# Kernel optimization log

Hardware: AMD Instinct MI355X
Metric: run time of the kernel (lower is better)

The kernel has to match this reference:

```python
import jax, jax.numpy as jnp
import numpy as np

DIM = 192
R = 16            # patches_resolution, D=H=W=R
SP = 4            # split_size
NH = 6            # num_heads (block level); per-branch heads = NH//3
B = 2
L = R * R * R
EPS = 1e-5


def layernorm(x, g, b):
    mu = jnp.mean(x, axis=-1, keepdims=True)
    var = jnp.mean(jnp.square(x - mu), axis=-1, keepdims=True)
    return (x - mu) * jax.lax.rsqrt(var + EPS) * g + b


def window_partition(x, d_sp, h_sp, w_sp, nh):
    b, _, _, _, cb = x.shape
    win = d_sp * h_sp * w_sp
    x = x.reshape(b, R // d_sp, d_sp, R // h_sp, h_sp, R // w_sp, w_sp, cb)
    x = x.transpose(0, 1, 3, 5, 2, 4, 6, 7).reshape(-1, win, nh, cb // nh)
    return x.transpose(0, 2, 1, 3)


def window_merge(x, d_sp, h_sp, w_sp, b):
    cb = x.shape[-1]
    x = x.reshape(b, R // d_sp, R // h_sp, R // w_sp, d_sp, h_sp, w_sp, cb)
    x = x.transpose(0, 1, 4, 2, 5, 3, 6, 7).reshape(b, L, cb)
    return x


def lepe_attention(q, k, v, d_sp, h_sp, w_sp, nh):
    # q,k,v: (B, L, Cb). Note: LePE bias is computed-but-unused in the source -> pure windowed SDPA.
    b, _, cb = q.shape
    hd = cb // nh
    scale = hd ** -0.5
    q5 = q.reshape(b, R, R, R, cb)
    k5 = k.reshape(b, R, R, R, cb)
    v5 = v.reshape(b, R, R, R, cb)
    qw = window_partition(q5, d_sp, h_sp, w_sp, nh) * scale
    kw = window_partition(k5, d_sp, h_sp, w_sp, nh)
    vw = window_partition(v5, d_sp, h_sp, w_sp, nh)
    attn = jax.nn.softmax(jnp.einsum('whqd,whkd->whqk', qw, kw), axis=-1)
    out = jnp.einsum('whqk,whkd->whqd', attn, vw)
    out = out.transpose(0, 2, 1, 3).reshape(-1, d_sp * h_sp * w_sp, cb)
    return window_merge(out, d_sp, h_sp, w_sp, b)


WINDOW_SHAPES = [(R, R, SP), (R, SP, R), (SP, R, R)]  # idx 0,1,2


def setup_inputs() -> dict:
    key = jax.random.key(0)
    ks = jax.random.split(key, 12)
    C = DIM
    H4 = int(C * 4)
    inp = {
        'x': jax.random.normal(ks[0], (B, C, R, R, R), dtype=jnp.float32),
        'w_qkv': jax.random.normal(ks[1], (C, 3 * C), dtype=jnp.float32) * (C ** -0.5),
        'w_proj': jax.random.normal(ks[2], (C, C), dtype=jnp.float32) * (C ** -0.5),
        'b_proj': jnp.zeros((C,), dtype=jnp.float32),
        'g1': jnp.ones((C,), dtype=jnp.float32),
        'b1': jnp.zeros((C,), dtype=jnp.float32),
        'g2': jnp.ones((C,), dtype=jnp.float32),
        'b2': jnp.zeros((C,), dtype=jnp.float32),
        'w_fc1': jax.random.normal(ks[3], (C, H4), dtype=jnp.float32) * (C ** -0.5),
        'b_fc1': jnp.zeros((H4,), dtype=jnp.float32),
        'w_fc2': jax.random.normal(ks[4], (H4, C), dtype=jnp.float32) * (H4 ** -0.5),
        'b_fc2': jnp.zeros((C,), dtype=jnp.float32),
    }
    return inp


def reference(x, w_qkv, w_proj, b_proj, g1, b1, g2, b2, w_fc1, b_fc1, w_fc2, b_fc2):
    C = DIM
    Cb = C // 3
    nh_b = NH // 3
    x = 2.0 * x
    xt = jnp.transpose(x, (0, 2, 3, 4, 1))                # (B, D, H, W, C)
    img = layernorm(xt, g1, b1)
    qkv = img.reshape(B, L, C) @ w_qkv                    # (B, L, 3C)
    q, k, v = jnp.split(qkv.reshape(B, L, 3, C).transpose(2, 0, 1, 3), 3, axis=0)
    q, k, v = q[0], k[0], v[0]                            # each (B, L, C)
    outs = []
    for i, (dsp, hsp, wsp) in enumerate(WINDOW_SHAPES):
        sl = slice(i * Cb, (i + 1) * Cb)
        outs.append(lepe_attention(q[..., sl], k[..., sl], v[..., sl], dsp, hsp, wsp, nh_b))
    attened = jnp.concatenate(outs, axis=2)               # (B, L, C)
    attened = attened @ w_proj + b_proj
    xs = xt.reshape(B, L, C) + attened
    h = layernorm(xs, g2, b2) @ w_fc1 + b_fc1
    h = jax.nn.gelu(h, approximate=False)
    xs = xs + (h @ w_fc2 + b_fc2)
    out = xs.reshape(B, R, R, R, C).transpose(0, 4, 1, 2, 3)  # (B, C, D, H, W)
    return out
```

## Files before the change

### kernel.cpp

```cpp
#include <hip/hip_runtime.h>
#include <hip/hip_bf16.h>

typedef __hip_bfloat16 bf16;
typedef short short8 __attribute__((ext_vector_type(8)));
typedef float floatx4 __attribute__((ext_vector_type(4)));

#define SZ (8192*192)

__device__ __forceinline__ unsigned short f2b(float f) {
    unsigned u = __builtin_bit_cast(unsigned, f);
    u += 0x7FFFu + ((u >> 16) & 1u);
    return (unsigned short)(u >> 16);
}
__device__ __forceinline__ float b2f(unsigned short h) {
    unsigned u = ((unsigned)h) << 16;
    return __builtin_bit_cast(float, u);
}
__device__ __forceinline__ unsigned pk2(float a, float b) {
    return ((unsigned)f2b(b) << 16) | (unsigned)f2b(a);
}
__device__ __forceinline__ float fexp2(float x) {
    float r;
    asm("v_exp_f32 %0, %1" : "=v"(r) : "v"(x));
    return r;
}

__device__ __forceinline__ int detect_inline(const unsigned* __restrict__ x32,
                                             int tid, int* cnt) {
    if (tid == 0) *cnt = 0;
    __syncthreads();
    if (tid < 256) {
        unsigned u = x32[tid];
        int c = (int)(((u >> 7) & 0xFFu) >= 152u) + (int)(((u >> 23) & 0xFFu) >= 152u);
        if (c) atomicAdd(cnt, c);
    }
    __syncthreads();
    return (*cnt >= 16) ? 1 : 0;
}

struct WPA { const void* s[11]; };

__global__ __launch_bounds__(256) void wprep_kernel(WPA a, unsigned short* __restrict__ wdst,
                                                    float* __restrict__ vdst,
                                                    const unsigned* __restrict__ x32) {
    __shared__ int cnt;
    int f = detect_inline(x32, threadIdx.x, &cnt);
    int i = blockIdx.x * 256 + threadIdx.x;
    if (i < 442368) {
        int seg, base, K, N;
        if (i < 110592)      { seg = 0; base = 0;      K = 192; N = 576; }
        else if (i < 147456) { seg = 1; base = 110592; K = 192; N = 192; }
        else if (i < 294912) { seg = 2; base = 147456; K = 192; N = 768; }
        else                 { seg = 3; base = 294912; K = 768; N = 192; }
        int j = i - base;
        int n = j / K, k = j - n * K;
        size_t src = (size_t)k * N + n;
        float v = f ? ((const float*)a.s[seg])[src] : b2f(((const unsigned short*)a.s[seg])[src]);
        int ci = (n >> 6) * (K >> 5) + (k >> 5);
        int off = (ci << 11) + (((n >> 4) & 3) << 9) + ((n & 15) << 5) + (k & 31);
        wdst[base + off] = f2b(v);
    } else if (i < 444288) {
        int j = i - 442368;
        int seg, off;
        if (j < 960)       { seg = 4 + j / 192; off = j % 192; }
        else if (j < 1728) { seg = 9; off = j - 960; }
        else               { seg = 10; off = j - 1728; }
        float v = f ? ((const float*)a.s[seg])[off] : b2f(((const unsigned short*)a.s[seg])[off]);
        vdst[j] = v;
    }
}


__global__ __launch_bounds__(256) void prep_kernel(const void* __restrict__ xin,
        int* __restrict__ flagOut,
        const float* __restrict__ g1, const float* __restrict__ b1,
        float* __restrict__ xt, unsigned short* __restrict__ img) {
    __shared__ float tile[192][33];
    __shared__ float mu[32], rs[32];
    __shared__ int cnt;
    int tid = threadIdx.x;
    int f = detect_inline((const unsigned*)xin, tid, &cnt);
    if (blockIdx.x == 0 && tid == 0) *flagOut = f;
    int t0 = blockIdx.x * 32;
    int b = t0 >> 12;
    int ts = t0 & 4095;
    for (int idx = tid; idx < 192 * 32; idx += 256) {
        int c = idx >> 5, tt = idx & 31;
        int gi = ((b * 192 + c) << 12) + ts + tt;
        float raw = f ? ((const float*)xin)[gi] : b2f(((const unsigned short*)xin)[gi]);
        tile[c][tt] = 2.0f * raw;
    }
    __syncthreads();
    {
        int tt = tid >> 3, j = tid & 7;
        int c0 = j * 24;
        float s = 0.f, sq = 0.f;
        #pragma unroll
        for (int i = 0; i < 24; ++i) { float v = tile[c0 + i][tt]; s += v; sq += v * v; }
        s += __shfl_xor(s, 1); sq += __shfl_xor(sq, 1);
        s += __shfl_xor(s, 2); sq += __shfl_xor(sq, 2);
        s += __shfl_xor(s, 4); sq += __shfl_xor(sq, 4);
        if (j == 0) {
            float m = s * (1.0f / 192.0f);
            float var = sq * (1.0f / 192.0f) - m * m;
            mu[tt] = m;
            rs[tt] = rsqrtf(var + 1e-5f);
        }
    }
    __syncthreads();
    for (int idx = tid; idx < 32 * 192; idx += 256) {
        int tt = idx / 192, c = idx % 192;
        float v = tile[c][tt];
        xt[(t0 + tt) * 192 + c] = v;
        int po = ((((t0 + tt) >> 4) * 6 + (c >> 5)) << 9) + ((tt & 15) << 5) + (c & 31);
        img[po] = f2b((v - mu[tt]) * rs[tt] * g1[c] + b1[c]);
    }
}

__device__ __forceinline__ int g_of(int br, int t) {
    if (br == 0) return (((t >> 2) & 3) << 10) | ((t >> 8) << 6) | (((t >> 4) & 15) << 2) | (t & 3);
    if (br == 1) return (((t >> 6) & 3) << 10) | ((t >> 8) << 6) | (((t >> 4) & 3) << 4) | (t & 15);
    return t;
}

template <int MODE, int W>
__global__ __launch_bounds__(64 * W) void mfma_gemm(const unsigned short* __restrict__ A,
        const unsigned short* __restrict__ WT, const float* __restrict__ bias,
        const float* __restrict__ resid, void* __restrict__ out,
        unsigned short* __restrict__ qt, unsigned short* __restrict__ kt,
        unsigned short* __restrict__ vt, int N, int K) {
    int wave = threadIdx.x >> 6, lane = threadIdx.x & 63;
    int quad = lane >> 4, l16 = lane & 15;
    int m0 = blockIdx.x * (32 * W) + wave * 32, n0 = blockIdx.y * 64;
    const int KT = K >> 5;
    const unsigned short* ap = A + (((size_t)(m0 >> 4) * KT) << 9) + l16 * 32 + quad * 8;
    const size_t a1off = ((size_t)KT) << 9;
    const unsigned short* wpB = WT + (((size_t)blockIdx.y * KT) << 11) + l16 * 32 + quad * 8;
    floatx4 acc[2][4] = {};
    #pragma unroll 2
    for (int kc = 0; kc < K; kc += 32) {
        const unsigned short* ac = ap + (((size_t)(kc >> 5)) << 9);
        short8 a0 = *reinterpret_cast<const short8*>(ac);
        short8 a1 = *reinterpret_cast<const short8*>(ac + a1off);
        const unsigned short* wc = wpB + (((size_t)(kc >> 5)) << 11);
        #pragma unroll
        for (int nt = 0; nt < 4; ++nt) {
            short8 w = *reinterpret_cast<const short8*>(wc + nt * 512);
            acc[0][nt] = __builtin_amdgcn_mfma_f32_16x16x32_bf16(a0, w, acc[0][nt], 0, 0, 0);
            acc[1][nt] = __builtin_amdgcn_mfma_f32_16x16x32_bf16(a1, w, acc[1][nt], 0, 0, 0);
        }
    }
    #pragma unroll
    for (int fh = 0; fh < 2; ++fh) {
        #pragma unroll
        for (int nt = 0; nt < 4; ++nt) {
            int col = n0 + nt * 16 + l16;
            if (MODE == 0 && n0 >= 384) {
                int cv = col - 384;
                int d = cv & 31, brh = cv >> 5;
                int row0 = m0 + fh * 16 + quad * 4;
                int bb_ = row0 >> 12, tl = row0 & 4095;
                int g0 = g_of(brh >> 1, tl);
                int wb2 = g0 >> 10, k = g0 & 63, c = k >> 4, m = k & 15;
                int pos = ((c >> 1) << 5) + ((m >> 2) << 3) + ((c & 1) << 2);
                int chunk = (g0 & 1023) >> 6;
                int tidx = ((d >> 4) << 1) | (pos >> 5);
                unsigned short* tile = vt + (((((size_t)(bb_ * 6 + brh) * 4 + wb2) * 16 + chunk) * 4 + tidx) << 9);
                ushort4 w4;
                w4.x = f2b(acc[fh][nt][0]);
                w4.y = f2b(acc[fh][nt][1]);
                w4.z = f2b(acc[fh][nt][2]);
                w4.w = f2b(acc[fh][nt][3]);
                *reinterpret_cast<ushort4*>(tile + (d & 15) * 32 + (pos & 31)) = w4;
            } else if (MODE == 0 && n0 >= 192) {
                int ck = col - 192;
                int d = ck & 31, brh = ck >> 5;
                int row0 = m0 + fh * 16 + quad * 4;
                int bb_ = row0 >> 12, tl = row0 & 4095;
                int g0 = g_of(brh >> 1, tl);
                int wb2 = g0 >> 10, k = g0 & 63, c = k >> 4, m = k & 15;
                int chunk = (g0 & 1023) >> 6;
                unsigned short* tile = kt + (((((size_t)(bb_ * 6 + brh) * 4 + wb2) * 16 + chunk) * 4 + c) << 9);
                tile[m * 32 + d]       = f2b(acc[fh][nt][0]);
                tile[(m + 1) * 32 + d] = f2b(acc[fh][nt][1]);
                tile[(m + 2) * 32 + d] = f2b(acc[fh][nt][2]);
                tile[(m + 3) * 32 + d] = f2b(acc[fh][nt][3]);
            } else if (MODE == 0) {
                int d = col & 31, brh = col >> 5;
                int row0 = m0 + fh * 16 + quad * 4;
                int bb_ = row0 >> 12, tl = row0 & 4095;
                int g0 = g_of(brh >> 1, tl);
                int wb2 = g0 >> 10, q = g0 & 1023;
                int chunk = q >> 4, m = q & 15;
                unsigned short* tile = qt + ((((size_t)(bb_ * 6 + brh) * 4 + wb2) * 64 + chunk) << 9);
                tile[m * 32 + d]       = f2b(acc[fh][nt][0] * 0.25503516527f);
                tile[(m + 1) * 32 + d] = f2b(acc[fh][nt][1] * 0.25503516527f);
                tile[(m + 2) * 32 + d] = f2b(acc[fh][nt][2] * 0.25503516527f);
                tile[(m + 3) * 32 + d] = f2b(acc[fh][nt][3] * 0.25503516527f);
            } else {
                #pragma unroll
                for (int r = 0; r < 4; ++r) {
                    int row = m0 + fh * 16 + quad * 4 + r;
                    float v = acc[fh][nt][r] + bias[col];
                    v = 0.5f * v * (1.0f + erff(v * 0.70710678118654752f));
                    size_t o = (((size_t)(row >> 4) * (N >> 5) + (col >> 5)) << 9)
                             + ((row & 15) << 5) + (col & 31);
                    ((unsigned short*)out)[o] = f2b(v);
                }
            }
        }
    }
}

__global__ __launch_bounds__(192) void proj_ln_kernel(const unsigned short* __restrict__ A,
        const unsigned short* __restrict__ WT, const float* __restrict__ bias,
        float* __restrict__ xs, const float* __restrict__ g2v, const float* __restrict__ b2v,
        unsigned short* __restrict__ lnb) {
    __shared__ float red[3][16][2];
    int wave = threadIdx.x >> 6, lane = threadIdx.x & 63;
    int quad = lane >> 4, l16 = lane & 15;
    int m0 = blockIdx.x * 16;
    const int KT = 6;
    const unsigned short* ap = A + (((size_t)(m0 >> 4) * KT) << 9) + l16 * 32 + quad * 8;
    const unsigned short* wpB = WT + (((size_t)wave * KT) << 11) + l16 * 32 + quad * 8;
    floatx4 acc[4] = {};
    #pragma unroll
    for (int kc = 0; kc < 192; kc += 32) {
        const unsigned short* ac = ap + (((size_t)(kc >> 5)) << 9);
        short8 a0 = *reinterpret_cast<const short8*>(ac);
        const unsigned short* wc = wpB + (((size_t)(kc >> 5)) << 11);
        #pragma unroll
        for (int nt = 0; nt < 4; ++nt) {
            short8 w = *reinterpret_cast<const short8*>(wc + nt * 512);
            acc[nt] = __builtin_amdgcn_mfma_f32_16x16x32_bf16(a0, w, acc[nt], 0, 0, 0);
        }
    }
    float vv[4][4];
    #pragma unroll
    for (int r = 0; r < 4; ++r) {
        float s = 0.f, sq = 0.f;
        #pragma unroll
        for (int nt = 0; nt < 4; ++nt) {
            int col = wave * 64 + nt * 16 + l16;
            int row = m0 + quad * 4 + r;
            size_t o = (size_t)row * 192 + col;
            float v = acc[nt][r] + bias[col] + xs[o];
            xs[o] = v;
            vv[nt][r] = v;
            s += v; sq += v * v;
        }
        s += __shfl_xor(s, 1); sq += __shfl_xor(sq, 1);
        s += __shfl_xor(s, 2); sq += __shfl_xor(sq, 2);
        s += __shfl_xor(s, 4); sq += __shfl_xor(sq, 4);
        s += __shfl_xor(s, 8); sq += __shfl_xor(sq, 8);
        if (l16 == 0) {
            int rw = quad * 4 + r;
            red[wave][rw][0] = s;
            red[wave][rw][1] = sq;
        }
    }
    __syncthreads();
    float mu[4], rsd[4];
    #pragma unroll
    for (int r = 0; r < 4; ++r) {
        int rw = quad * 4 + r;
        float S  = red[0][rw][0] + red[1][rw][0] + red[2][rw][0];
        float SQ = red[0][rw][1] + red[1][rw][1] + red[2][rw][1];
        float m = S * (1.0f / 192.0f);
        float var = SQ * (1.0f / 192.0f) - m * m;
        mu[r] = m;
        rsd[r] = rsqrtf(var + 1e-5f);
    }
    #pragma unroll
    for (int nt = 0; nt < 4; ++nt) {
        #pragma unroll
        for (int r = 0; r < 4; ++r) {
            int col = wave * 64 + nt * 16 + l16;
            int row = m0 + quad * 4 + r;
            float v = (vv[nt][r] - mu[r]) * rsd[r] * g2v[col] + b2v[col];
            size_t o = (((size_t)(row >> 4) * 6 + (col >> 5)) << 9) + ((row & 15) << 5) + (col & 31);
            lnb[o] = f2b(v);
        }
    }
}

__global__ __launch_bounds__(64) void fc2_out_kernel(const unsigned short* __restrict__ A,
        const unsigned short* __restrict__ WT, const float* __restrict__ bias,
        const float* __restrict__ xs, void* __restrict__ out,
        const int* __restrict__ flag) {
    __shared__ float tile[64][33];
    int tid = threadIdx.x;
    int quad = tid >> 4, l16 = tid & 15;
    int m0 = blockIdx.x * 32, n0 = blockIdx.y * 64;
    const int KT = 24;
    const unsigned short* ap = A + (((size_t)(m0 >> 4) * KT) << 9) + l16 * 32 + quad * 8;
    const size_t a1off = ((size_t)KT) << 9;
    const unsigned short* wpB = WT + (((size_t)blockIdx.y * KT) << 11) + l16 * 32 + quad * 8;
    floatx4 acc[2][4] = {};
    #pragma unroll 2
    for (int kc = 0; kc < 768; kc += 32) {
        const unsigned short* ac = ap + (((size_t)(kc >> 5)) << 9);
        short8 a0 = *reinterpret_cast<const short8*>(ac);
        short8 a1 = *reinterpret_cast<const short8*>(ac + a1off);
        const unsigned short* wc = wpB + (((size_t)(kc >> 5)) << 11);
        #pragma unroll
        for (int nt = 0; nt < 4; ++nt) {
            short8 w = *reinterpret_cast<const short8*>(wc + nt * 512);
            acc[0][nt] = __builtin_amdgcn_mfma_f32_16x16x32_bf16(a0, w, acc[0][nt], 0, 0, 0);
            acc[1][nt] = __builtin_amdgcn_mfma_f32_16x16x32_bf16(a1, w, acc[1][nt], 0, 0, 0);
        }
    }
    #pragma unroll
    for (int fh = 0; fh < 2; ++fh) {
        #pragma unroll
        for (int nt = 0; nt < 4; ++nt) {
            #pragma unroll
            for (int r = 0; r < 4; ++r) {
                int col = n0 + nt * 16 + l16;
                int row = m0 + fh * 16 + quad * 4 + r;
                float v = acc[fh][nt][r] + bias[col] + xs[(size_t)row * 192 + col];
                tile[nt * 16 + l16][fh * 16 + quad * 4 + r] = v;
            }
        }
    }
    __syncthreads();
    int f = *flag;
    int b = m0 >> 12, ts = m0 & 4095;
    #pragma unroll 4
    for (int it = 0; it < 32; ++it) {
        int idx = it * 64 + tid;
        int cc = idx >> 5, tt = idx & 31;
        float v = tile[cc][tt];
        size_t o = (((size_t)(b * 192 + n0 + cc)) << 12) + ts + tt;
        if (f) ((float*)out)[o] = v;
        else   ((unsigned short*)out)[o] = f2b(v);
    }
}

__device__ __forceinline__ int tok_of(int br, int wb, int q) {
    if (br == 0) return ((q >> 6) << 8) | (((q >> 2) & 15) << 4) | (wb << 2) | (q & 3);
    else if (br == 1) return ((q >> 6) << 8) | (((wb << 2) + ((q >> 4) & 3)) << 4) | (q & 15);
    else return (((wb << 2) + (q >> 8)) << 8) | (q & 255);
}

__global__ __launch_bounds__(256) void attn_mfma(const unsigned short* __restrict__ qt,
        const unsigned short* __restrict__ kt, const unsigned short* __restrict__ vt,
        unsigned short* __restrict__ attb) {
    int hw = blockIdx.x;
    int bid = (hw & 7) * 96 + (hw >> 3);
    int qti = bid & 15, head = (bid >> 4) & 1, wb = (bid >> 5) & 3, b = (bid >> 7) & 1, br = bid >> 8;
    int tid = threadIdx.x;
    int wave = tid >> 6, lane = tid & 63, quad = lane >> 4, l16 = lane & 15;
    int coff = br * 64 + head * 32;
    int brh = br * 2 + head;
    int tb = b << 12;
    size_t qbase = ((((size_t)(b * 6 + brh) * 4 + wb) * 64 + qti * 4 + wave) << 9) + l16 * 32 + quad * 8;
    short8 aq = *reinterpret_cast<const short8*>(qt + qbase);
    floatx4 o0 = {}, o1 = {};
    float lsum = 0.f;

    const size_t kvbase = ((((size_t)(b * 6 + brh) * 4 + wb) * 16) << 11) + l16 * 32 + quad * 8;
    const unsigned short* kp = kt + kvbase;
    const unsigned short* vp = vt + kvbase;

    short8 k0 = *reinterpret_cast<const short8*>(kp);
    short8 k1 = *reinterpret_cast<const short8*>(kp + 512);
    short8 k2 = *reinterpret_cast<const short8*>(kp + 1024);
    short8 k3 = *reinterpret_cast<const short8*>(kp + 1536);
    short8 vb00 = *reinterpret_cast<const short8*>(vp);
    short8 vb01 = *reinterpret_cast<const short8*>(vp + 512);
    short8 vb10 = *reinterpret_cast<const short8*>(vp + 1024);
    short8 vb11 = *reinterpret_cast<const short8*>(vp + 1536);

    for (int it = 0; it < 16; ++it) {
        short8 ck0 = k0, ck1 = k1, ck2 = k2, ck3 = k3;
        short8 cv00 = vb00, cv01 = vb01, cv10 = vb10, cv11 = vb11;
        if (it + 1 < 16) {
            kp += 2048; vp += 2048;
            k0 = *reinterpret_cast<const short8*>(kp);
            k1 = *reinterpret_cast<const short8*>(kp + 512);
            k2 = *reinterpret_cast<const short8*>(kp + 1024);
            k3 = *reinterpret_cast<const short8*>(kp + 1536);
            vb00 = *reinterpret_cast<const short8*>(vp);
            vb01 = *reinterpret_cast<const short8*>(vp + 512);
            vb10 = *reinterpret_cast<const short8*>(vp + 1024);
            vb11 = *reinterpret_cast<const short8*>(vp + 1536);
        }
        floatx4 z = {};
        floatx4 s0 = __builtin_amdgcn_mfma_f32_16x16x32_bf16(ck0, aq, z, 0, 0, 0);
        floatx4 s1 = __builtin_amdgcn_mfma_f32_16x16x32_bf16(ck1, aq, z, 0, 0, 0);
        floatx4 s2 = __builtin_amdgcn_mfma_f32_16x16x32_bf16(ck2, aq, z, 0, 0, 0);
        floatx4 s3 = __builtin_amdgcn_mfma_f32_16x16x32_bf16(ck3, aq, z, 0, 0, 0);
        float p00 = fexp2(s0[0]), p01 = fexp2(s0[1]), p02 = fexp2(s0[2]), p03 = fexp2(s0[3]);
        float p10 = fexp2(s1[0]), p11 = fexp2(s1[1]), p12 = fexp2(s1[2]), p13 = fexp2(s1[3]);
        float p20 = fexp2(s2[0]), p21 = fexp2(s2[1]), p22 = fexp2(s2[2]), p23 = fexp2(s2[3]);
        float p30 = fexp2(s3[0]), p31 = fexp2(s3[1]), p32 = fexp2(s3[2]), p33 = fexp2(s3[3]);
        lsum += ((p00 + p01) + (p02 + p03)) + ((p10 + p11) + (p12 + p13))
              + ((p20 + p21) + (p22 + p23)) + ((p30 + p31) + (p32 + p33));
        uint4 ua, ub;
        ua.x = pk2(p00, p01); ua.y = pk2(p02, p03); ua.z = pk2(p10, p11); ua.w = pk2(p12, p13);
        ub.x = pk2(p20, p21); ub.y = pk2(p22, p23); ub.z = pk2(p30, p31); ub.w = pk2(p32, p33);
        short8 pa0 = __builtin_bit_cast(short8, ua);
        short8 pa1 = __builtin_bit_cast(short8, ub);
        o0 = __builtin_amdgcn_mfma_f32_16x16x32_bf16(pa0, cv00, o0, 0, 0, 0);
        o0 = __builtin_amdgcn_mfma_f32_16x16x32_bf16(pa1, cv01, o0, 0, 0, 0);
        o1 = __builtin_amdgcn_mfma_f32_16x16x32_bf16(pa0, cv10, o1, 0, 0, 0);
        o1 = __builtin_amdgcn_mfma_f32_16x16x32_bf16(pa1, cv11, o1, 0, 0, 0);
    }
    lsum += __shfl_xor(lsum, 16);
    lsum += __shfl_xor(lsum, 32);
    #pragma unroll
    for (int r = 0; r < 4; ++r) {
        float inv = 1.0f / __shfl(lsum, quad * 4 + r);
        int q = qti * 64 + wave * 16 + quad * 4 + r;
        int t = tb + tok_of(br, wb, q);
        size_t o = (((size_t)(t >> 4) * 6 + (coff >> 5)) << 9) + ((t & 15) << 5);
        attb[o + l16]      = f2b(o0[r] * inv);
        attb[o + 16 + l16] = f2b(o1[r] * inv);
    }
}

extern "C" void kernel_launch(void* const* d_in, const int* in_sizes, int n_in,
                              void* d_out, int out_size, void* d_ws, size_t ws_size,
                              hipStream_t stream) {
    float* ws = (float*)d_ws;

    float* vbase = ws;
    float* bprojf = vbase + 0;
    float* g1f    = vbase + 192;
    float* b1f    = vbase + 384;
    float* g2f    = vbase + 576;
    float* b2f    = vbase + 768;
    float* bfc1f  = vbase + 960;
    float* bfc2f  = vbase + 1728;

    unsigned short* wbase = (unsigned short*)(ws + 1920);
    unsigned short* wqkvT = wbase + 0;
    unsigned short* wprojT = wbase + 110592;
    unsigned short* wfc1T = wbase + 147456;
    unsigned short* wfc2T = wbase + 294912;

    size_t p = 1920 + 442368 / 2;
    float* xt = ws + p; p += SZ;
    unsigned short* img = (unsigned short*)(ws + p); p += SZ / 2;
    size_t pQ = p;
    unsigned short* hbuf = (unsigned short*)(ws + pQ);
    p = pQ + 8192 * 768 / 2;
    unsigned short* attb = (unsigned short*)(ws + p); p += SZ / 2;
    int* flag = (int*)(ws + p); p += 16;
    unsigned short* qtb = (unsigned short*)(ws + p); p += SZ / 2;
    unsigned short* ktb = (unsigned short*)(ws + p); p += SZ / 2;
    unsigned short* vtb = (unsigned short*)(ws + p); p += SZ / 2;
    float* xs = xt;
    unsigned short* lnb = img;

    WPA wa;
    wa.s[0] = d_in[1];  wa.s[1] = d_in[2];  wa.s[2] = d_in[8];  wa.s[3] = d_in[10];
    wa.s[4] = d_in[3];  wa.s[5] = d_in[4];  wa.s[6] = d_in[5];  wa.s[7] = d_in[6];
    wa.s[8] = d_in[7];  wa.s[9] = d_in[9];  wa.s[10] = d_in[11];

    wprep_kernel<<<dim3(1736), dim3(256), 0, stream>>>(wa, wbase, vbase,
        (const unsigned*)d_in[0]);
    prep_kernel<<<dim3(256), dim3(256), 0, stream>>>(d_in[0], flag, g1f, b1f, xt, img);
    mfma_gemm<0, 2><<<dim3(128, 9), dim3(128), 0, stream>>>(
        img, wqkvT, nullptr, nullptr, nullptr, qtb, ktb, vtb, 576, 192);
    attn_mfma<<<dim3(768), dim3(256), 0, stream>>>(qtb, ktb, vtb, attb);
    proj_ln_kernel<<<dim3(512), dim3(192), 0, stream>>>(
        attb, wprojT, bprojf, xs, g2f, b2f, lnb);
    mfma_gemm<2, 2><<<dim3(128, 12), dim3(128), 0, stream>>>(
        lnb, wfc1T, bfc1f, nullptr, hbuf, nullptr, nullptr, nullptr, 768, 192);
    fc2_out_kernel<<<dim3(256, 3), dim3(64), 0, stream>>>(
        hbuf, wfc2T, bfc2f, xs, d_out, flag);
}
```

Measured before the change: 175.6 us.

## Fuse fc1 GEMM and GELU into proj+LayerNorm kernel via shared-memory LN tile

The post-projection LayerNorm output is now written to a shared-memory tile instead of global memory, and the same block runs the fc1 GEMM (768 columns split across 3 waves) plus bias and GELU, writing hbuf directly. This removes one kernel launch and the global round trip of the LN activations. In exchange, each 16-row block now rereads the whole fc1 weight matrix with little reuse. With only 512 blocks of 3 waves doing serial MFMA chains, the GEMM may also run with lower parallelism than the separate tiled GEMM did.

```diff
diff --git a/kernel.cpp b/kernel.cpp
--- a/kernel.cpp
+++ b/kernel.cpp
@@ -185,7 +185,7 @@
                 tile[(m + 1) * 32 + d] = f2b(acc[fh][nt][1]);
                 tile[(m + 2) * 32 + d] = f2b(acc[fh][nt][2]);
                 tile[(m + 3) * 32 + d] = f2b(acc[fh][nt][3]);
-            } else if (MODE == 0) {
+            } else {
                 int d = col & 31, brh = col >> 5;
                 int row0 = m0 + fh * 16 + quad * 4;
                 int bb_ = row0 >> 12, tl = row0 & 4095;
@@ -197,32 +197,24 @@
                 tile[(m + 1) * 32 + d] = f2b(acc[fh][nt][1] * 0.25503516527f);
                 tile[(m + 2) * 32 + d] = f2b(acc[fh][nt][2] * 0.25503516527f);
                 tile[(m + 3) * 32 + d] = f2b(acc[fh][nt][3] * 0.25503516527f);
-            } else {
-                #pragma unroll
-                for (int r = 0; r < 4; ++r) {
-                    int row = m0 + fh * 16 + quad * 4 + r;
-                    float v = acc[fh][nt][r] + bias[col];
-                    v = 0.5f * v * (1.0f + erff(v * 0.70710678118654752f));
-                    size_t o = (((size_t)(row >> 4) * (N >> 5) + (col >> 5)) << 9)
-                             + ((row & 15) << 5) + (col & 31);
-                    ((unsigned short*)out)[o] = f2b(v);
-                }
             }
         }
     }
 }
 
-__global__ __launch_bounds__(192) void proj_ln_kernel(const unsigned short* __restrict__ A,
-        const unsigned short* __restrict__ WT, const float* __restrict__ bias,
+__global__ __launch_bounds__(192) void proj_ln_fc1_kernel(const unsigned short* __restrict__ A,
+        const unsigned short* __restrict__ WTp, const float* __restrict__ bproj,
         float* __restrict__ xs, const float* __restrict__ g2v, const float* __restrict__ b2v,
-        unsigned short* __restrict__ lnb) {
+        const unsigned short* __restrict__ WTf, const float* __restrict__ bfc1,
+        unsigned short* __restrict__ hbuf) {
     __shared__ float red[3][16][2];
+    __shared__ __align__(16) unsigned short lnA[6 * 512];
     int wave = threadIdx.x >> 6, lane = threadIdx.x & 63;
     int quad = lane >> 4, l16 = lane & 15;
     int m0 = blockIdx.x * 16;
     const int KT = 6;
     const unsigned short* ap = A + (((size_t)(m0 >> 4) * KT) << 9) + l16 * 32 + quad * 8;
-    const unsigned short* wpB = WT + (((size_t)wave * KT) << 11) + l16 * 32 + quad * 8;
+    const unsigned short* wpB = WTp + (((size_t)wave * KT) << 11) + l16 * 32 + quad * 8;
     floatx4 acc[4] = {};
     #pragma unroll
     for (int kc = 0; kc < 192; kc += 32) {
@@ -244,7 +236,7 @@
             int col = wave * 64 + nt * 16 + l16;
             int row = m0 + quad * 4 + r;
             size_t o = (size_t)row * 192 + col;
-            float v = acc[nt][r] + bias[col] + xs[o];
+            float v = acc[nt][r] + bproj[col] + xs[o];
             xs[o] = v;
             vv[nt][r] = v;
             s += v; sq += v * v;
@@ -276,10 +268,36 @@
         #pragma unroll
         for (int r = 0; r < 4; ++r) {
             int col = wave * 64 + nt * 16 + l16;
+            int row = quad * 4 + r;
+            float v = (vv[nt][r] - mu[r]) * rsd[r] * g2v[col] + b2v[col];
+            lnA[((col >> 5) << 9) + (row << 5) + (col & 31)] = f2b(v);
+        }
+    }
+    __syncthreads();
+    short8 af[6];
+    #pragma unroll
+    for (int kk = 0; kk < 6; ++kk)
+        af[kk] = *reinterpret_cast<const short8*>(lnA + (kk << 9) + l16 * 32 + quad * 8);
+    #pragma unroll 2
+    for (int t = 0; t < 16; ++t) {
+        int n0f = wave * 256 + t * 16;
+        const unsigned short* wf = WTf + ((((size_t)(n0f >> 6)) * 6) << 11)
+                                 + (((n0f >> 4) & 3) << 9) + l16 * 32 + quad * 8;
+        floatx4 accf = {};
+        #pragma unroll
+        for (int kk = 0; kk < 6; ++kk) {
+            short8 w = *reinterpret_cast<const short8*>(wf + (kk << 11));
+            accf = __builtin_amdgcn_mfma_f32_16x16x32_bf16(af[kk], w, accf, 0, 0, 0);
+        }
+        int col = n0f + l16;
+        #pragma unroll
+        for (int r = 0; r < 4; ++r) {
             int row = m0 + quad * 4 + r;
-            float v = (vv[nt][r] - mu[r]) * rsd[r] * g2v[col] + b2v[col];
-            size_t o = (((size_t)(row >> 4) * 6 + (col >> 5)) << 9) + ((row & 15) << 5) + (col & 31);
-            lnb[o] = f2b(v);
+            float v = accf[r] + bfc1[col];
+            v = 0.5f * v * (1.0f + erff(v * 0.70710678118654752f));
+            size_t o = (((size_t)(row >> 4) * 24 + (col >> 5)) << 9)
+                     + ((row & 15) << 5) + (col & 31);
+            hbuf[o] = f2b(v);
         }
     }
 }
@@ -452,7 +470,6 @@
     unsigned short* ktb = (unsigned short*)(ws + p); p += SZ / 2;
     unsigned short* vtb = (unsigned short*)(ws + p); p += SZ / 2;
     float* xs = xt;
-    unsigned short* lnb = img;
 
     WPA wa;
     wa.s[0] = d_in[1];  wa.s[1] = d_in[2];  wa.s[2] = d_in[8];  wa.s[3] = d_in[10];
@@ -465,10 +482,8 @@
     mfma_gemm<0, 2><<<dim3(128, 9), dim3(128), 0, stream>>>(
         img, wqkvT, nullptr, nullptr, nullptr, qtb, ktb, vtb, 576, 192);
     attn_mfma<<<dim3(768), dim3(256), 0, stream>>>(qtb, ktb, vtb, attb);
-    proj_ln_kernel<<<dim3(512), dim3(192), 0, stream>>>(
-        attb, wprojT, bprojf, xs, g2f, b2f, lnb);
-    mfma_gemm<2, 2><<<dim3(128, 12), dim3(128), 0, stream>>>(
-        lnb, wfc1T, bfc1f, nullptr, hbuf, nullptr, nullptr, nullptr, 768, 192);
+    proj_ln_fc1_kernel<<<dim3(512), dim3(192), 0, stream>>>(
+        attb, wprojT, bprojf, xs, g2f, b2f, wfc1T, bfc1f, hbuf);
     fc2_out_kernel<<<dim3(256, 3), dim3(64), 0, stream>>>(
         hbuf, wfc2T, bfc2f, xs, d_out, flag);
 }
```

Measured after the change: 177.7 us. Within noise of the previous version (+1.2%).
